# Performance work log

Measured on AMD Instinct MI355X. Metric: run time of the kernel, lower is better.

Reference implementation:

```python
import jax, jax.numpy as jnp
import numpy as np

V, D, Z, C = 50000, 300, 128, 10

def setup_inputs() -> dict:
    key = jax.random.key(0)
    ks = jax.random.split(key, 12)
    idxs = jax.random.randint(ks[0], (C,), 0, V)
    center_idx = jax.random.randint(ks[1], (), 0, V)
    center_word = jnp.zeros((V,), jnp.float32).at[center_idx].set(1.0)  # one-hot [V]
    context_words = jnp.zeros((C, V), jnp.float32).at[jnp.arange(C), idxs].set(1.0)  # one-hot [C,V]
    s = 0.05
    return {
        "center_word": center_word,
        "context_words": context_words,
        "context_word_idxs": idxs,
        "eps": jax.random.normal(ks[2], (Z,), jnp.float32),
        "E": jax.random.normal(ks[3], (D, V), jnp.float32) * s,
        "W_mu": jax.random.normal(ks[4], (Z, 2 * D), jnp.float32) * s,
        "b_mu": jnp.zeros((Z,), jnp.float32),
        "W_sig": jax.random.normal(ks[5], (Z, 2 * D), jnp.float32) * s,
        "b_sig": jnp.zeros((Z,), jnp.float32),
        "prior_mean": jax.random.normal(ks[6], (Z, V), jnp.float32) * s,
        "prior_sigma": jax.random.normal(ks[7], (Z, V), jnp.float32) * s,
        "W_gen": jax.random.normal(ks[8], (V, Z), jnp.float32) * s,
        "b_gen": jnp.zeros((V,), jnp.float32),
    }


def reference(center_word, context_words, context_word_idxs, eps,
              E, W_mu, b_mu, W_sig, b_sig, prior_mean, prior_sigma, W_gen, b_gen):
    # One-hot matmul 'lookups' (faithful to original dense matmuls)
    ce = center_word @ E.T                      # [D]
    cw = context_words @ E.T                    # [C, D]
    cat = jnp.concatenate([jnp.broadcast_to(ce, (cw.shape[0], ce.shape[0])), cw], axis=1)  # [C, 2D]
    summed = jax.nn.relu(cat).sum(0)            # [2D]
    u = W_mu @ summed + b_mu                    # [Z]
    s = jax.nn.softplus(W_sig @ summed + b_sig)  # [Z]
    z = u + eps * s                             # reparameterized sample [Z]
    logprobs = jax.nn.log_softmax(W_gen @ z + b_gen)  # [V]
    # prior (note: original computes z_mean but never uses it in the KL)
    z_sigma = jax.nn.softplus(center_word @ prior_sigma.T)  # [Z]
    loss_probs = logprobs[context_word_idxs]    # gather [C]
    kl = jnp.log(z_sigma / s) + (s**2 + (u - z_sigma) ** 2) / (2.0 * z_sigma**2) - 0.5
    return loss_probs.sum() - kl.sum()
```

## Files before the change

### kernel.cpp

```cpp
#include <hip/hip_runtime.h>
#include <float.h>
#include <math.h>

#define V 50000
#define D 300
#define Z 128
#define C 10
#define TWOD 600
#define NENC 32
#define RWE 8
#define RPB 64
#define NCON 782
#define FINAL_BID (NENC + NCON)
#define NBLK (FINAL_BID + 1)
#define NREP 16
#define MAGIC 0x5F3C7A91u

typedef unsigned long long u64;


__device__ __forceinline__ float softplusf(float x) {
    return log1pf(expf(-fabsf(x))) + fmaxf(x, 0.0f);
}
__device__ __forceinline__ void st_u32(unsigned* p, unsigned v) {
    __hip_atomic_store(p, v, __ATOMIC_RELAXED, __HIP_MEMORY_SCOPE_AGENT);
}
__device__ __forceinline__ unsigned ld_u32(const unsigned* p) {
    return __hip_atomic_load(p, __ATOMIC_RELAXED, __HIP_MEMORY_SCOPE_AGENT);
}
__device__ __forceinline__ u64 ld_u64(const u64* p) {
    return __hip_atomic_load(p, __ATOMIC_RELAXED, __HIP_MEMORY_SCOPE_AGENT);
}
__device__ __forceinline__ void st_tag(u64* p, float x) {
    u64 v = ((u64)MAGIC << 32) | (u64)__float_as_uint(x);
    __hip_atomic_store(p, v, __ATOMIC_RELAXED, __HIP_MEMORY_SCOPE_AGENT);
}
__device__ __forceinline__ float poll_tag(u64* p) {
    u64 v;
    for (;;) {
        v = __hip_atomic_load(p, __ATOMIC_RELAXED, __HIP_MEMORY_SCOPE_AGENT);
        if ((unsigned)(v >> 32) == MAGIC) break;
        __builtin_amdgcn_s_sleep(1);
    }
    return __uint_as_float((unsigned)v);
}
__device__ __forceinline__ float finish_tag(u64 v, u64* p) {
    return ((unsigned)(v >> 32) == MAGIC) ? __uint_as_float((unsigned)v)
                                          : poll_tag(p);
}
__device__ __forceinline__ void gload16(const void* g, void* l) {
    __builtin_amdgcn_global_load_lds(
        (const __attribute__((address_space(1))) void*)g,
        (__attribute__((address_space(3))) void*)l,
        16, 0, 0);
}

__global__ __launch_bounds__(256, 4) void k_all(
        const float* __restrict__ cw,
        const float* __restrict__ E,
        const int* __restrict__ idxs,
        const float* __restrict__ Wmu, const float* __restrict__ bmu,
        const float* __restrict__ Wsig, const float* __restrict__ bsig,
        const float* __restrict__ eps,
        const float* __restrict__ psig,
        const float* __restrict__ Wgen, const float* __restrict__ bgen,
        char* __restrict__ ws, float* __restrict__ out) {
    unsigned* cidx_enc = (unsigned*)(ws + 0);
    u64*      rawtag   = (u64*)(ws + 4096);
    u64*      bmbs     = (u64*)(ws + 270336);
    u64*      gslots   = (u64*)(ws + 286720);
    u64*      klslot   = (u64*)(ws + 290816);

    __shared__ __align__(16) float wtile[RPB * Z];
    __shared__ float summed[TWOD];
    __shared__ float rawv[2 * Z];
    __shared__ __align__(16) float zsh[Z];
    __shared__ float lsh[RPB];
    __shared__ float bgsh[RPB];
    __shared__ int sidx[C];
    __shared__ float red_m[4], red_s[4], klred[2];
    __shared__ int scidx;

    int bid = blockIdx.x, tid = threadIdx.x;
    int w = tid >> 6, l = tid & 63;
    if (tid < C) sidx[tid] = idxs[tid];

    if (bid < NENC) {
        int r0 = bid * RWE + w * 2, r1 = r0 + 1;
        const float* W0; const float* W1; float b0, b1;
        if (r0 < Z) { W0 = Wmu + (size_t)r0 * TWOD;        b0 = bmu[r0]; }
        else        { W0 = Wsig + (size_t)(r0 - Z) * TWOD; b0 = bsig[r0 - Z]; }
        if (r1 < Z) { W1 = Wmu + (size_t)r1 * TWOD;        b1 = bmu[r1]; }
        else        { W1 = Wsig + (size_t)(r1 - Z) * TWOD; b1 = bsig[r1 - Z]; }

        float w0c[5], w1c[5];
        #pragma unroll
        for (int i = 0; i < 5; ++i) {
            int k = l + i * 64;
            w0c[i] = (k < D) ? W0[k] : 0.0f;
            w1c[i] = (k < D) ? W1[k] : 0.0f;
        }
        __syncthreads();
        for (int d = tid; d < D; d += 256) {
            float acc = 0.0f;
            #pragma unroll
            for (int c = 0; c < C; ++c)
                acc += fmaxf(E[(size_t)d * V + sidx[c]], 0.0f);
            summed[D + d] = acc;
        }
        __syncthreads();
        float p0 = 0.0f, p1 = 0.0f;
        for (int k = l; k < D; k += 64) {
            float s = summed[D + k];
            p0 += W0[D + k] * s;
            p1 += W1[D + k] * s;
        }
        if (tid == 0) {
            unsigned e;
            for (;;) {
                e = ld_u32(cidx_enc);
                if (e - MAGIC < (unsigned)V) break;
                __builtin_amdgcn_s_sleep(1);
            }
            scidx = (int)(e - MAGIC);
        }
        __syncthreads();
        int cidx = scidx;
        for (int d = tid; d < D; d += 256)
            summed[d] = (float)C * fmaxf(E[(size_t)d * V + cidx], 0.0f);
        __syncthreads();
        #pragma unroll
        for (int i = 0; i < 5; ++i) {
            int k = l + i * 64;
            if (k < D) {
                float s = summed[k];
                p0 += w0c[i] * s;
                p1 += w1c[i] * s;
            }
        }
        #pragma unroll
        for (int off = 32; off; off >>= 1) {
            p0 += __shfl_xor(p0, off);
            p1 += __shfl_xor(p1, off);
        }
        float val0 = p0 + b0, val1 = p1 + b1;
        if (l < 32) {
            int rep = l & 15;
            int r   = (l < 16) ? r0 : r1;
            float v = (l < 16) ? val0 : val1;
            st_tag(rawtag + (size_t)(rep * 256 + r) * 8, v);
        }
        return;
    }

    if (bid == FINAL_BID) {
        u64 vm[4], vs[4];
        #pragma unroll
        for (int i = 0; i < 4; ++i) {
            int t = tid + i * 256;
            if (t < NCON) {
                vm[i] = ld_u64(bmbs + 2 * (size_t)t);
                vs[i] = ld_u64(bmbs + 2 * (size_t)t + 1);
            }
        }
        float fm = -FLT_MAX, fs = 0.0f;
        #pragma unroll
        for (int i = 0; i < 4; ++i) {
            int t = tid + i * 256;
            if (t < NCON) {
                float m2 = finish_tag(vm[i], bmbs + 2 * (size_t)t);
                float s2 = finish_tag(vs[i], bmbs + 2 * (size_t)t + 1);
                float M = fmaxf(fm, m2);
                fs = fs * expf(fm - M) + s2 * expf(m2 - M);
                fm = M;
            }
        }
        #pragma unroll
        for (int off = 32; off; off >>= 1) {
            float m2 = __shfl_xor(fm, off), s2 = __shfl_xor(fs, off);
            float M = fmaxf(fm, m2);
            fs = fs * expf(fm - M) + s2 * expf(m2 - M);
            fm = M;
        }
        if (l == 0) { red_m[w] = fm; red_s[w] = fs; }
        __syncthreads();
        if (tid == 0) {
            float M = red_m[0], S = red_s[0];
            #pragma unroll
            for (int w2 = 1; w2 < 4; ++w2) {
                float m2 = red_m[w2], s2 = red_s[w2];
                float Mn = fmaxf(M, m2);
                S = S * expf(M - Mn) + s2 * expf(m2 - Mn);
                M = Mn;
            }
            float lse = M + logf(S);
            float g = 0.0f;
            #pragma unroll
            for (int c = 0; c < C; ++c) g += poll_tag(gslots + (size_t)c * 8);
            float kls = poll_tag(klslot);
            out[0] = g - (float)C * lse - kls;
        }
        return;
    }

    int c = bid - NENC;
    int g = c * 256 + tid;
    if (g < V / 4) {
        float4 wv = ((const float4*)cw)[g];
        int found = -1;
        if      (wv.x != 0.0f) found = 4 * g + 0;
        else if (wv.y != 0.0f) found = 4 * g + 1;
        else if (wv.z != 0.0f) found = 4 * g + 2;
        else if (wv.w != 0.0f) found = 4 * g + 3;
        if (found >= 0) st_u32(cidx_enc, (unsigned)found + MAGIC);
    }

    int base = c * RPB;
    {
        const char* gw = (const char*)Wgen + ((size_t)base + (size_t)w * 16) * 512;
        #pragma unroll
        for (int i = 0; i < 8; ++i) {
            int row0 = base + w * 16 + 2 * i;
            const char* src = (row0 + 2 <= V) ? gw + i * 1024
                                              : (const char*)Wgen;
            gload16(src + l * 16, &wtile[w * 2048 + i * 256]);
        }
    }
    if (tid < RPB) {
        int rr = base + tid;
        bgsh[tid] = bgen[rr < V ? rr : V - 1];
    }
    float ev = (tid < Z) ? eps[tid] : 0.0f;

    rawv[tid] = poll_tag(rawtag + (size_t)((bid & (NREP - 1)) * 256 + tid) * 8);
    if (c == 0 && tid == 0) {
        unsigned e;
        for (;;) {
            e = ld_u32(cidx_enc);
            if (e - MAGIC < (unsigned)V) break;
            __builtin_amdgcn_s_sleep(1);
        }
        scidx = (int)(e - MAGIC);
    }
    __syncthreads();

    if (tid < Z) {
        float u = rawv[tid];
        float s = softplusf(rawv[Z + tid]);
        zsh[tid] = u + ev * s;
        if (c == 0) {
            float zs = softplusf(psig[(size_t)tid * V + scidx]);
            float kl = logf(zs / s) + (s * s + (u - zs) * (u - zs)) / (2.0f * zs * zs) - 0.5f;
            #pragma unroll
            for (int off = 32; off; off >>= 1) kl += __shfl_xor(kl, off);
            if (l == 0) klred[w] = kl;
        }
    }
    __syncthreads();
    if (c == 0 && tid == 0) st_tag(klslot, klred[0] + klred[1]);

    asm volatile("s_waitcnt vmcnt(0)" ::: "memory");
    float4 zreg = ((const float4*)zsh)[l & 31];
    #pragma unroll
    for (int i = 0; i < 8; ++i) {
        const float4 wv = *(const float4*)&wtile[w * 2048 + i * 256
                                                 + (l >> 5) * 128 + (l & 31) * 4];
        float p = wv.x * zreg.x + wv.y * zreg.y + wv.z * zreg.z + wv.w * zreg.w;
        p += __shfl_xor(p, 1);  p += __shfl_xor(p, 2);  p += __shfl_xor(p, 4);
        p += __shfl_xor(p, 8);  p += __shfl_xor(p, 16);
        if ((l & 31) == 0) {
            int rloc = w * 16 + 2 * i + (l >> 5);
            int row = base + rloc;
            lsh[rloc] = (row < V) ? (p + bgsh[rloc]) : -FLT_MAX;
        }
    }
    __syncthreads();

    if (w == 0) {
        float lg = lsh[l];
        float m = lg, s = (lg > -FLT_MAX) ? 1.0f : 0.0f;
        #pragma unroll
        for (int off = 32; off; off >>= 1) {
            float m2 = __shfl_xor(m, off), s2 = __shfl_xor(s, off);
            float M = fmaxf(m, m2);
            s = s * expf(m - M) + s2 * expf(m2 - M);
            m = M;
        }
        if (l == 0) {
            st_tag(bmbs + 2 * (size_t)c, m);
            st_tag(bmbs + 2 * (size_t)c + 1, s);
        }
    }
    if (tid < RPB) {
        int row = base + tid;
        if (row < V) {
            float lg = lsh[tid];
            #pragma unroll
            for (int cc = 0; cc < C; ++cc)
                if (row == sidx[cc]) st_tag(gslots + (size_t)cc * 8, lg);
        }
    }
}

extern "C" void kernel_launch(void* const* d_in, const int* in_sizes, int n_in,
                              void* d_out, int out_size, void* d_ws, size_t ws_size,
                              hipStream_t stream) {
    const float* center = (const float*)d_in[0];
    const int*   idxs   = (const int*)d_in[2];
    const float* eps    = (const float*)d_in[3];
    const float* E      = (const float*)d_in[4];
    const float* Wmu    = (const float*)d_in[5];
    const float* bmu    = (const float*)d_in[6];
    const float* Wsig   = (const float*)d_in[7];
    const float* bsig   = (const float*)d_in[8];
    const float* psig   = (const float*)d_in[10];
    const float* Wgen   = (const float*)d_in[11];
    const float* bgen   = (const float*)d_in[12];

    k_all<<<NBLK, 256, 0, stream>>>(center, E, idxs, Wmu, bmu, Wsig, bsig,
                                    eps, psig, Wgen, bgen,
                                    (char*)d_ws, (float*)d_out);
}
```

Measured before the change: 14.22 us.

## Move z/KL computation into encoder blocks and double rows per consumer block

Encoder blocks now compute u, softplus sigma, the sampled z and per-block KL partial sums themselves, publishing z values (replicated) instead of raw encoder outputs. Consumer blocks just poll z, so they skip per-block softplus and the block-0 KL serial path. Rows per consumer block go from 64 to 128, halving the block count and the number of partial max/sum records the final block reduces. The final block gathers KL partials and gathered logits in parallel instead of polling serially. The cost is more LDS per block, lower occupancy (launch bounds 2), and encoder blocks now depend on the center index.

```diff
diff --git a/kernel.cpp b/kernel.cpp
--- a/kernel.cpp
+++ b/kernel.cpp
@@ -8,9 +8,8 @@
 #define C 10
 #define TWOD 600
 #define NENC 32
-#define RWE 8
-#define RPB 64
-#define NCON 782
+#define RPB 128
+#define NCON 391
 #define FINAL_BID (NENC + NCON)
 #define NBLK (FINAL_BID + 1)
 #define NREP 16
@@ -55,7 +54,7 @@
         16, 0, 0);
 }
 
-__global__ __launch_bounds__(256, 4) void k_all(
+__global__ __launch_bounds__(256, 2) void k_all(
         const float* __restrict__ cw,
         const float* __restrict__ E,
         const int* __restrict__ idxs,
@@ -66,19 +65,20 @@
         const float* __restrict__ Wgen, const float* __restrict__ bgen,
         char* __restrict__ ws, float* __restrict__ out) {
     unsigned* cidx_enc = (unsigned*)(ws + 0);
-    u64*      rawtag   = (u64*)(ws + 4096);
-    u64*      bmbs     = (u64*)(ws + 270336);
-    u64*      gslots   = (u64*)(ws + 286720);
-    u64*      klslot   = (u64*)(ws + 290816);
+    u64*      ztag     = (u64*)(ws + 4096);
+    u64*      bmbs     = (u64*)(ws + 139264);
+    u64*      gslots   = (u64*)(ws + 167936);
+    u64*      klpart   = (u64*)(ws + 169984);
 
     __shared__ __align__(16) float wtile[RPB * Z];
     __shared__ float summed[TWOD];
-    __shared__ float rawv[2 * Z];
     __shared__ __align__(16) float zsh[Z];
     __shared__ float lsh[RPB];
     __shared__ float bgsh[RPB];
+    __shared__ float uv[8], zsh_e[4], klsh[4];
+    __shared__ float gsh[16];
     __shared__ int sidx[C];
-    __shared__ float red_m[4], red_s[4], klred[2];
+    __shared__ float red_m[4], red_s[4], klred[1];
     __shared__ int scidx;
 
     int bid = blockIdx.x, tid = threadIdx.x;
@@ -86,12 +86,14 @@
     if (tid < C) sidx[tid] = idxs[tid];
 
     if (bid < NENC) {
-        int r0 = bid * RWE + w * 2, r1 = r0 + 1;
-        const float* W0; const float* W1; float b0, b1;
-        if (r0 < Z) { W0 = Wmu + (size_t)r0 * TWOD;        b0 = bmu[r0]; }
-        else        { W0 = Wsig + (size_t)(r0 - Z) * TWOD; b0 = bsig[r0 - Z]; }
-        if (r1 < Z) { W1 = Wmu + (size_t)r1 * TWOD;        b1 = bmu[r1]; }
-        else        { W1 = Wsig + (size_t)(r1 - Z) * TWOD; b1 = bsig[r1 - Z]; }
+        int jbase = bid * 4;
+        bool isMu = (w < 2);
+        int j0 = jbase + (w & 1) * 2;
+        const float* Wb = isMu ? Wmu : Wsig;
+        const float* bb = isMu ? bmu : bsig;
+        const float* W0 = Wb + (size_t)j0 * TWOD;
+        const float* W1 = W0 + TWOD;
+        float b0 = bb[j0], b1 = bb[j0 + 1];
 
         float w0c[5], w1c[5];
         #pragma unroll
@@ -143,37 +145,54 @@
             p0 += __shfl_xor(p0, off);
             p1 += __shfl_xor(p1, off);
         }
-        float val0 = p0 + b0, val1 = p1 + b1;
-        if (l < 32) {
-            int rep = l & 15;
-            int r   = (l < 16) ? r0 : r1;
-            float v = (l < 16) ? val0 : val1;
-            st_tag(rawtag + (size_t)(rep * 256 + r) * 8, v);
+        if (l == 0) {
+            int u0 = (isMu ? 0 : 4) + (w & 1) * 2;
+            uv[u0]     = p0 + b0;
+            uv[u0 + 1] = p1 + b1;
+        }
+        __syncthreads();
+        if (tid < 4) {
+            float u  = uv[tid];
+            float s  = softplusf(uv[4 + tid]);
+            zsh_e[tid] = u + eps[jbase + tid] * s;
+            float zs = softplusf(psig[(size_t)(jbase + tid) * V + cidx]);
+            klsh[tid] = logf(zs / s)
+                      + (s * s + (u - zs) * (u - zs)) / (2.0f * zs * zs) - 0.5f;
+        }
+        __syncthreads();
+        if (tid < 64) {
+            int rep = tid & 15, j = tid >> 4;
+            st_tag(ztag + (size_t)(rep * 128 + jbase + j) * 8, zsh_e[j]);
+        } else if (tid == 64) {
+            st_tag(klpart + (size_t)bid * 8, klsh[0] + klsh[1] + klsh[2] + klsh[3]);
         }
         return;
     }
 
     if (bid == FINAL_BID) {
-        u64 vm[4], vs[4];
-        #pragma unroll
-        for (int i = 0; i < 4; ++i) {
-            int t = tid + i * 256;
-            if (t < NCON) {
-                vm[i] = ld_u64(bmbs + 2 * (size_t)t);
-                vs[i] = ld_u64(bmbs + 2 * (size_t)t + 1);
-            }
-        }
+        int t0 = tid, t1 = tid + 256;
+        u64 vm0 = 0, vs0 = 0, vm1 = 0, vs1 = 0, kv = 0, gv = 0;
+        if (t0 < NCON) { vm0 = ld_u64(bmbs + (size_t)t0 * 8);
+                         vs0 = ld_u64(bmbs + (size_t)t0 * 8 + 1); }
+        if (t1 < NCON) { vm1 = ld_u64(bmbs + (size_t)t1 * 8);
+                         vs1 = ld_u64(bmbs + (size_t)t1 * 8 + 1); }
+        if (tid < 32)  kv = ld_u64(klpart + (size_t)tid * 8);
+        if (tid < C)   gv = ld_u64(gslots + (size_t)tid * 8);
+
         float fm = -FLT_MAX, fs = 0.0f;
-        #pragma unroll
-        for (int i = 0; i < 4; ++i) {
-            int t = tid + i * 256;
-            if (t < NCON) {
-                float m2 = finish_tag(vm[i], bmbs + 2 * (size_t)t);
-                float s2 = finish_tag(vs[i], bmbs + 2 * (size_t)t + 1);
-                float M = fmaxf(fm, m2);
-                fs = fs * expf(fm - M) + s2 * expf(m2 - M);
-                fm = M;
-            }
+        if (t0 < NCON) {
+            float m2 = finish_tag(vm0, bmbs + (size_t)t0 * 8);
+            float s2 = finish_tag(vs0, bmbs + (size_t)t0 * 8 + 1);
+            float M = fmaxf(fm, m2);
+            fs = fs * expf(fm - M) + s2 * expf(m2 - M);
+            fm = M;
+        }
+        if (t1 < NCON) {
+            float m2 = finish_tag(vm1, bmbs + (size_t)t1 * 8);
+            float s2 = finish_tag(vs1, bmbs + (size_t)t1 * 8 + 1);
+            float M = fmaxf(fm, m2);
+            fs = fs * expf(fm - M) + s2 * expf(m2 - M);
+            fm = M;
         }
         #pragma unroll
         for (int off = 32; off; off >>= 1) {
@@ -183,6 +202,13 @@
             fm = M;
         }
         if (l == 0) { red_m[w] = fm; red_s[w] = fs; }
+        float kp = (tid < 32) ? finish_tag(kv, klpart + (size_t)tid * 8) : 0.0f;
+        if (w == 0) {
+            #pragma unroll
+            for (int off = 32; off; off >>= 1) kp += __shfl_xor(kp, off);
+            if (l == 0) klred[0] = kp;
+        }
+        if (tid < C) gsh[tid] = finish_tag(gv, gslots + (size_t)tid * 8);
         __syncthreads();
         if (tid == 0) {
             float M = red_m[0], S = red_s[0];
@@ -196,9 +222,8 @@
             float lse = M + logf(S);
             float g = 0.0f;
             #pragma unroll
-            for (int c = 0; c < C; ++c) g += poll_tag(gslots + (size_t)c * 8);
-            float kls = poll_tag(klslot);
-            out[0] = g - (float)C * lse - kls;
+            for (int c = 0; c < C; ++c) g += gsh[c];
+            out[0] = g - (float)C * lse - klred[0];
         }
         return;
     }
@@ -217,59 +242,34 @@
 
     int base = c * RPB;
     {
-        const char* gw = (const char*)Wgen + ((size_t)base + (size_t)w * 16) * 512;
-        #pragma unroll
-        for (int i = 0; i < 8; ++i) {
-            int row0 = base + w * 16 + 2 * i;
+        const char* gw = (const char*)Wgen + ((size_t)base + (size_t)w * 32) * 512;
+        #pragma unroll
+        for (int i = 0; i < 16; ++i) {
+            int row0 = base + w * 32 + 2 * i;
             const char* src = (row0 + 2 <= V) ? gw + i * 1024
                                               : (const char*)Wgen;
-            gload16(src + l * 16, &wtile[w * 2048 + i * 256]);
+            gload16(src + l * 16, &wtile[w * 4096 + i * 256]);
         }
     }
     if (tid < RPB) {
         int rr = base + tid;
         bgsh[tid] = bgen[rr < V ? rr : V - 1];
     }
-    float ev = (tid < Z) ? eps[tid] : 0.0f;
-
-    rawv[tid] = poll_tag(rawtag + (size_t)((bid & (NREP - 1)) * 256 + tid) * 8);
-    if (c == 0 && tid == 0) {
-        unsigned e;
-        for (;;) {
-            e = ld_u32(cidx_enc);
-            if (e - MAGIC < (unsigned)V) break;
-            __builtin_amdgcn_s_sleep(1);
-        }
-        scidx = (int)(e - MAGIC);
-    }
+    if (tid < Z)
+        zsh[tid] = poll_tag(ztag + (size_t)((c & (NREP - 1)) * 128 + tid) * 8);
     __syncthreads();
-
-    if (tid < Z) {
-        float u = rawv[tid];
-        float s = softplusf(rawv[Z + tid]);
-        zsh[tid] = u + ev * s;
-        if (c == 0) {
-            float zs = softplusf(psig[(size_t)tid * V + scidx]);
-            float kl = logf(zs / s) + (s * s + (u - zs) * (u - zs)) / (2.0f * zs * zs) - 0.5f;
-            #pragma unroll
-            for (int off = 32; off; off >>= 1) kl += __shfl_xor(kl, off);
-            if (l == 0) klred[w] = kl;
-        }
-    }
-    __syncthreads();
-    if (c == 0 && tid == 0) st_tag(klslot, klred[0] + klred[1]);
 
     asm volatile("s_waitcnt vmcnt(0)" ::: "memory");
     float4 zreg = ((const float4*)zsh)[l & 31];
     #pragma unroll
-    for (int i = 0; i < 8; ++i) {
-        const float4 wv = *(const float4*)&wtile[w * 2048 + i * 256
+    for (int i = 0; i < 16; ++i) {
+        const float4 wv = *(const float4*)&wtile[w * 4096 + i * 256
                                                  + (l >> 5) * 128 + (l & 31) * 4];
         float p = wv.x * zreg.x + wv.y * zreg.y + wv.z * zreg.z + wv.w * zreg.w;
         p += __shfl_xor(p, 1);  p += __shfl_xor(p, 2);  p += __shfl_xor(p, 4);
         p += __shfl_xor(p, 8);  p += __shfl_xor(p, 16);
         if ((l & 31) == 0) {
-            int rloc = w * 16 + 2 * i + (l >> 5);
+            int rloc = w * 32 + 2 * i + (l >> 5);
             int row = base + rloc;
             lsh[rloc] = (row < V) ? (p + bgsh[rloc]) : -FLT_MAX;
         }
@@ -277,8 +277,9 @@
     __syncthreads();
 
     if (w == 0) {
-        float lg = lsh[l];
-        float m = lg, s = (lg > -FLT_MAX) ? 1.0f : 0.0f;
+        float a = lsh[l], b = lsh[l + 64];
+        float m = fmaxf(a, b);
+        float s = expf(a - m) + ((b > -FLT_MAX) ? expf(b - m) : 0.0f);
         #pragma unroll
         for (int off = 32; off; off >>= 1) {
             float m2 = __shfl_xor(m, off), s2 = __shfl_xor(s, off);
@@ -287,8 +288,8 @@
             m = M;
         }
         if (l == 0) {
-            st_tag(bmbs + 2 * (size_t)c, m);
-            st_tag(bmbs + 2 * (size_t)c + 1, s);
+            st_tag(bmbs + (size_t)c * 8, m);
+            st_tag(bmbs + (size_t)c * 8 + 1, s);
         }
     }
     if (tid < RPB) {
```

New measurement: 17.51 us. 23.1% more time.
